# Kernel tuning notes

Hardware: AMD Instinct MI355X
Metric: run time of the kernel (lower is better)

Reference implementation:

```python
import jax, jax.numpy as jnp
import numpy as np

EPS_BN = 1e-5
EPS_NORM = 1e-12
TOP_K = 512


def _conv(x, w):
    # NCHW conv, stride 1, SAME padding (ultralytics Conv autopad)
    return jax.lax.conv_general_dilated(x, w, (1, 1), 'SAME',
                                        dimension_numbers=('NCHW', 'OIHW', 'NCHW'))


def _bn(x, g, b, m, v):
    # inference-mode BatchNorm2d
    inv = jax.lax.rsqrt(v + EPS_BN)
    return (x - m[None, :, None, None]) * (g * inv)[None, :, None, None] + b[None, :, None, None]


def _descriptor(feat, p):
    (w_dr, g_dr, b_dr, m_dr, v_dr,
     w_d1, g_d1, b_d1, m_d1, v_d1,
     g_e, b_e, m_e, v_e,
     w_d2, g_d2, b_d2, m_d2, v_d2) = p
    # dim_reduce: Conv(channel, channel//2, 1) = conv+BN+SiLU
    x = jax.nn.silu(_bn(_conv(feat, w_dr), g_dr, b_dr, m_dr, v_dr))
    # descriptor: Conv(c/2, c/2, 3) + BN + ReLU + Conv(c/2, c/4, 1)
    x = jax.nn.silu(_bn(_conv(x, w_d1), g_d1, b_d1, m_d1, v_d1))
    x = jax.nn.relu(_bn(x, g_e, b_e, m_e, v_e))
    x = jax.nn.silu(_bn(_conv(x, w_d2), g_d2, b_d2, m_d2, v_d2))
    return x


def _keypoints(desc):
    b, c, h, w = desc.shape
    resp = jnp.sqrt(jnp.sum(desc * desc, axis=1)).reshape(b, h * w)  # L2 norm over channels
    _, idx = jax.lax.top_k(resp, TOP_K)                              # [b, K]
    y = (idx // w).astype(desc.dtype) / (h - 1) * 2 - 1
    x = (idx % w).astype(desc.dtype) / (w - 1) * 2 - 1
    return jnp.stack([x, y], axis=-1), idx                           # [b,K,2], [b,K]


def _forward(rgb_feat, ir_feat, params):
    rgb_desc = _descriptor(rgb_feat, params)
    ir_desc = _descriptor(ir_feat, params)

    kp1, idx1 = _keypoints(rgb_desc)
    kp2, idx2 = _keypoints(ir_desc)

    b, c, h, w = rgb_desc.shape
    hw = h * w
    d1 = rgb_desc.reshape(b, c, hw)
    d2 = ir_desc.reshape(b, c, hw)
    d1 = d1 / jnp.maximum(jnp.linalg.norm(d1, axis=1, keepdims=True), EPS_NORM)
    d2 = d2 / jnp.maximum(jnp.linalg.norm(d2, axis=1, keepdims=True), EPS_NORM)
    corr = jnp.einsum('bcn,bcm->bnm', d1, d2)     # [b, hw, hw]
    soft = jax.nn.softmax(corr, axis=-1)

    # scalar matching weight per keypoint pair (gather at keypoint locations)
    bidx = jnp.arange(b)[:, None]
    wts = soft[bidx, idx1, idx2]                  # [b, K]

    # vectorized DLT: A rows, two per point, weighted
    x1, y1 = kp1[..., 0], kp1[..., 1]
    x2, y2 = kp2[..., 0], kp2[..., 1]
    one = jnp.ones_like(x1)
    zer = jnp.zeros_like(x1)
    r1 = jnp.stack([x1, y1, one, zer, zer, zer, -x2 * x1, -x2 * y1, -x2], axis=-1)
    r2 = jnp.stack([zer, zer, zer, x1, y1, one, -y2 * x1, -y2 * y1, -y2], axis=-1)
    A = jnp.stack([r1, r2], axis=2) * wts[:, :, None, None]   # [b,K,2,9]
    A = A.reshape(b, 2 * TOP_K, 9)

    _, _, Vh = jnp.linalg.svd(A, full_matrices=False)          # Vh: [b,9,9]
    # torch.svd returns V; original takes V[-1] == last COLUMN of jax Vh
    H = Vh[:, :, -1].reshape(b, 3, 3)
    return H, rgb_desc, ir_desc


def setup_inputs() -> dict:
    key = jax.random.key(0)
    ks = jax.random.split(key, 8)
    B, C, Hh, Ww = 2, 256, 64, 64
    c2, c4 = C // 2, C // 4
    f32 = jnp.float32

    def bn_params(c):
        return (jnp.ones((c,), f32), jnp.zeros((c,), f32),
                jnp.zeros((c,), f32), jnp.ones((c,), f32))

    g_dr, b_dr, m_dr, v_dr = bn_params(c2)
    g_d1, b_d1, m_d1, v_d1 = bn_params(c2)
    g_e, b_e, m_e, v_e = bn_params(c2)
    g_d2, b_d2, m_d2, v_d2 = bn_params(c4)

    return {
        'rgb_feat': jax.random.normal(ks[0], (B, C, Hh, Ww), f32),
        'ir_feat': jax.random.normal(ks[1], (B, C, Hh, Ww), f32),
        'w_dr': jax.random.normal(ks[2], (c2, C, 1, 1), f32) * 0.05,
        'g_dr': g_dr, 'b_dr': b_dr, 'm_dr': m_dr, 'v_dr': v_dr,
        'w_d1': jax.random.normal(ks[3], (c2, c2, 3, 3), f32) * 0.05,
        'g_d1': g_d1, 'b_d1': b_d1, 'm_d1': m_d1, 'v_d1': v_d1,
        'g_e': g_e, 'b_e': b_e, 'm_e': m_e, 'v_e': v_e,
        'w_d2': jax.random.normal(ks[4], (c4, c2, 1, 1), f32) * 0.05,
        'g_d2': g_d2, 'b_d2': b_d2, 'm_d2': m_d2, 'v_d2': v_d2,
    }


def reference(rgb_feat, ir_feat,
              w_dr, g_dr, b_dr, m_dr, v_dr,
              w_d1, g_d1, b_d1, m_d1, v_d1,
              g_e, b_e, m_e, v_e,
              w_d2, g_d2, b_d2, m_d2, v_d2):
    params = (w_dr, g_dr, b_dr, m_dr, v_dr,
              w_d1, g_d1, b_d1, m_d1, v_d1,
              g_e, b_e, m_e, v_e,
              w_d2, g_d2, b_d2, m_d2, v_d2)
    return _forward(rgb_feat, ir_feat, params)
```

## Files before the change

### kernel.cpp

```cpp
#include <hip/hip_runtime.h>
#include <math.h>


#define HW4 4096
#define NIMG 4

#define OFF_X1   0L
#define OFF_X2   (OFF_X1 + 4L*128*4096)
#define OFF_RESP (OFF_X2 + 4L*128*4096)
#define OFF_INVN (OFF_RESP + 4L*4096)
#define OFF_TOPI (OFF_INVN + 4L*4096)
#define OFF_WTS  (OFF_TOPI + 4L*512)
#define OFF_A    (OFF_WTS + 2L*512)
#define OFF_QN   OFF_X1
#define OFF_PART (OFF_X1 + 65536L)

#define NSPLIT 16

__device__ __forceinline__ float silu_f(float y) { return y / (1.f + expf(-y)); }

__global__ __launch_bounds__(256) void fm_conv1(
    const float* __restrict__ rgb, const float* __restrict__ ir,
    const float* __restrict__ w, const float* __restrict__ g,
    const float* __restrict__ bb, const float* __restrict__ mm,
    const float* __restrict__ vv, float* __restrict__ x1) {
  __shared__ float wl[256*8];
  int bid = blockIdx.x;
  int pblk = bid & 3, ocg = (bid >> 2) & 15, img = bid >> 6;
  int oc0 = ocg * 8;
  int tid = threadIdx.x;
  const float* src = (img < 2) ? (rgb + (long)img*256*HW4) : (ir + (long)(img-2)*256*HW4);
  for (int i = tid; i < 2048; i += 256) {
    int o = i & 7, ic = i >> 3;
    wl[i] = w[(oc0 + o)*256 + ic];
  }
  __syncthreads();
  int p0 = pblk*1024 + tid*4;
  float acc[8][4];
  #pragma unroll
  for (int o = 0; o < 8; ++o)
    #pragma unroll
    for (int j = 0; j < 4; ++j) acc[o][j] = 0.f;
  #pragma unroll 4
  for (int ic = 0; ic < 256; ++ic) {
    float4 v = *(const float4*)(src + (long)ic*HW4 + p0);
    float4 wa = *(const float4*)&wl[ic*8];
    float4 wb = *(const float4*)&wl[ic*8 + 4];
    acc[0][0] = fmaf(wa.x, v.x, acc[0][0]); acc[0][1] = fmaf(wa.x, v.y, acc[0][1]);
    acc[0][2] = fmaf(wa.x, v.z, acc[0][2]); acc[0][3] = fmaf(wa.x, v.w, acc[0][3]);
    acc[1][0] = fmaf(wa.y, v.x, acc[1][0]); acc[1][1] = fmaf(wa.y, v.y, acc[1][1]);
    acc[1][2] = fmaf(wa.y, v.z, acc[1][2]); acc[1][3] = fmaf(wa.y, v.w, acc[1][3]);
    acc[2][0] = fmaf(wa.z, v.x, acc[2][0]); acc[2][1] = fmaf(wa.z, v.y, acc[2][1]);
    acc[2][2] = fmaf(wa.z, v.z, acc[2][2]); acc[2][3] = fmaf(wa.z, v.w, acc[2][3]);
    acc[3][0] = fmaf(wa.w, v.x, acc[3][0]); acc[3][1] = fmaf(wa.w, v.y, acc[3][1]);
    acc[3][2] = fmaf(wa.w, v.z, acc[3][2]); acc[3][3] = fmaf(wa.w, v.w, acc[3][3]);
    acc[4][0] = fmaf(wb.x, v.x, acc[4][0]); acc[4][1] = fmaf(wb.x, v.y, acc[4][1]);
    acc[4][2] = fmaf(wb.x, v.z, acc[4][2]); acc[4][3] = fmaf(wb.x, v.w, acc[4][3]);
    acc[5][0] = fmaf(wb.y, v.x, acc[5][0]); acc[5][1] = fmaf(wb.y, v.y, acc[5][1]);
    acc[5][2] = fmaf(wb.y, v.z, acc[5][2]); acc[5][3] = fmaf(wb.y, v.w, acc[5][3]);
    acc[6][0] = fmaf(wb.z, v.x, acc[6][0]); acc[6][1] = fmaf(wb.z, v.y, acc[6][1]);
    acc[6][2] = fmaf(wb.z, v.z, acc[6][2]); acc[6][3] = fmaf(wb.z, v.w, acc[6][3]);
    acc[7][0] = fmaf(wb.w, v.x, acc[7][0]); acc[7][1] = fmaf(wb.w, v.y, acc[7][1]);
    acc[7][2] = fmaf(wb.w, v.z, acc[7][2]); acc[7][3] = fmaf(wb.w, v.w, acc[7][3]);
  }
  #pragma unroll
  for (int o = 0; o < 8; ++o) {
    int oc = oc0 + o;
    float inv = 1.f / sqrtf(vv[oc] + 1e-5f);
    float sc = g[oc]*inv;
    float4 r;
    r.x = silu_f((acc[o][0] - mm[oc])*sc + bb[oc]);
    r.y = silu_f((acc[o][1] - mm[oc])*sc + bb[oc]);
    r.z = silu_f((acc[o][2] - mm[oc])*sc + bb[oc]);
    r.w = silu_f((acc[o][3] - mm[oc])*sc + bb[oc]);
    *(float4*)(x1 + ((long)img*128 + oc)*HW4 + p0) = r;
  }
}

#define C3_TW 72
#define C3_TR 18
__global__ __launch_bounds__(256) void fm_conv3(
    const float* __restrict__ x1, const float* __restrict__ w,
    const float* __restrict__ g1, const float* __restrict__ b1,
    const float* __restrict__ m1, const float* __restrict__ v1,
    const float* __restrict__ ge, const float* __restrict__ be,
    const float* __restrict__ me, const float* __restrict__ ve,
    float* __restrict__ x2) {
  __shared__ float t[2][4][C3_TR*C3_TW];
  __shared__ float wl[2][4][9][8];
  int bid = blockIdx.x;
  int rt = bid & 3, ocg = (bid >> 2) & 15, img = bid >> 6;
  int oc0 = ocg * 8;
  int y0 = rt * 16;
  int tid = threadIdx.x;
  int ly = tid >> 4;
  int lx = tid & 15;
  int x0 = lx * 4;
  const float* xim = x1 + (long)img*128*HW4;

  int gbase[5][4];
  int lofs[5];
  #pragma unroll
  for (int t5 = 0; t5 < 5; ++t5) {
    int i = tid + 256*t5;
    if (i < 1224) {
      int q = i / 306, r = i - q*306;
      int row = r / 17, seg = r - row*17;
      int gy = y0 + row - 1;
      lofs[t5] = q*(C3_TR*C3_TW) + row*C3_TW + 4 + seg*4;
      #pragma unroll
      for (int e = 0; e < 4; ++e) {
        int x = seg*4 + e - 1;
        gbase[t5][e] = (gy >= 0 && gy < 64 && x >= 0 && x < 64)
                       ? (q*HW4 + gy*64 + x) : -1;
      }
    } else {
      lofs[t5] = -1;
      #pragma unroll
      for (int e = 0; e < 4; ++e) gbase[t5][e] = -1;
    }
  }
  int wg0 = -1, wl0 = 0, wg1 = -1, wl1 = 0;
  {
    int i = tid;
    if (i < 288) {
      int o = i & 7, k = (i >> 3) % 9, q = i / 72;
      wg0 = ((oc0 + o)*128 + q)*9 + k;
      wl0 = (q*9 + k)*8 + o;
    }
    i = tid + 256;
    if (i < 288) {
      int o = i & 7, k = (i >> 3) % 9, q = i / 72;
      wg1 = ((oc0 + o)*128 + q)*9 + k;
      wl1 = (q*9 + k)*8 + o;
    }
  }

  float4 sreg[5];
  float wreg0 = 0.f, wreg1 = 0.f;

  #define C3_LOAD(IC0) do {                                              \
    long icoff = (long)(IC0)*HW4;                                        \
    _Pragma("unroll")                                                    \
    for (int t5 = 0; t5 < 5; ++t5) {                                     \
      sreg[t5].x = (gbase[t5][0] >= 0) ? xim[icoff + gbase[t5][0]] : 0.f;\
      sreg[t5].y = (gbase[t5][1] >= 0) ? xim[icoff + gbase[t5][1]] : 0.f;\
      sreg[t5].z = (gbase[t5][2] >= 0) ? xim[icoff + gbase[t5][2]] : 0.f;\
      sreg[t5].w = (gbase[t5][3] >= 0) ? xim[icoff + gbase[t5][3]] : 0.f;\
    }                                                                    \
    if (wg0 >= 0) wreg0 = w[(long)(IC0)*9 + wg0];                        \
    if (wg1 >= 0) wreg1 = w[(long)(IC0)*9 + wg1];                        \
  } while (0)

  #define C3_WRITE(BUF) do {                                             \
    float* tb = &t[BUF][0][0];                                           \
    _Pragma("unroll")                                                    \
    for (int t5 = 0; t5 < 5; ++t5)                                       \
      if (lofs[t5] >= 0) *(float4*)(tb + lofs[t5]) = sreg[t5];           \
    if (wg0 >= 0) (&wl[BUF][0][0][0])[wl0] = wreg0;                      \
    if (wg1 >= 0) (&wl[BUF][0][0][0])[wl1] = wreg1;                      \
  } while (0)

  float acc[8][4];
  #pragma unroll
  for (int o = 0; o < 8; ++o)
    #pragma unroll
    for (int j = 0; j < 4; ++j) acc[o][j] = 0.f;

  C3_LOAD(0);
  C3_WRITE(0);
  __syncthreads();
  int pb = 0;
  for (int ic0 = 0; ic0 < 128; ic0 += 4) {
    if (ic0 + 4 < 128) C3_LOAD(ic0 + 4);
    #pragma unroll
    for (int q = 0; q < 4; ++q) {
      const float* tq = &t[pb][q][0];
      float n6[3][6];
      #pragma unroll
      for (int dy = 0; dy < 3; ++dy) {
        float4 a = *(const float4*)(tq + (ly + dy)*C3_TW + x0 + 4);
        float4 b2 = *(const float4*)(tq + (ly + dy)*C3_TW + x0 + 8);
        n6[dy][0] = a.x; n6[dy][1] = a.y; n6[dy][2] = a.z;
        n6[dy][3] = a.w; n6[dy][4] = b2.x; n6[dy][5] = b2.y;
      }
      #pragma unroll
      for (int k = 0; k < 9; ++k) {
        const int dy = k / 3, dx = k % 3;
        float4 wA = *(const float4*)&wl[pb][q][k][0];
        float4 wB = *(const float4*)&wl[pb][q][k][4];
        #pragma unroll
        for (int j = 0; j < 4; ++j) {
          float nv = n6[dy][dx + j];
          acc[0][j] = fmaf(wA.x, nv, acc[0][j]);
          acc[1][j] = fmaf(wA.y, nv, acc[1][j]);
          acc[2][j] = fmaf(wA.z, nv, acc[2][j]);
          acc[3][j] = fmaf(wA.w, nv, acc[3][j]);
          acc[4][j] = fmaf(wB.x, nv, acc[4][j]);
          acc[5][j] = fmaf(wB.y, nv, acc[5][j]);
          acc[6][j] = fmaf(wB.z, nv, acc[6][j]);
          acc[7][j] = fmaf(wB.w, nv, acc[7][j]);
        }
      }
    }
    if (ic0 + 4 < 128) C3_WRITE(pb ^ 1);
    __syncthreads();
    pb ^= 1;
  }
  int prow = (y0 + ly)*64 + x0;
  #pragma unroll
  for (int o = 0; o < 8; ++o) {
    int oc = oc0 + o;
    float inv1 = 1.f / sqrtf(v1[oc] + 1e-5f);
    float s1 = g1[oc]*inv1;
    float inve = 1.f / sqrtf(ve[oc] + 1e-5f);
    float s2 = ge[oc]*inve;
    float4 r;
    float y;
    y = silu_f((acc[o][0] - m1[oc])*s1 + b1[oc]); r.x = fmaxf((y - me[oc])*s2 + be[oc], 0.f);
    y = silu_f((acc[o][1] - m1[oc])*s1 + b1[oc]); r.y = fmaxf((y - me[oc])*s2 + be[oc], 0.f);
    y = silu_f((acc[o][2] - m1[oc])*s1 + b1[oc]); r.z = fmaxf((y - me[oc])*s2 + be[oc], 0.f);
    y = silu_f((acc[o][3] - m1[oc])*s1 + b1[oc]); r.w = fmaxf((y - me[oc])*s2 + be[oc], 0.f);
    *(float4*)(x2 + ((long)img*128 + oc)*HW4 + prow) = r;
  }
}

__global__ __launch_bounds__(256) void fm_conv2(
    const float* __restrict__ x2, const float* __restrict__ w,
    const float* __restrict__ g, const float* __restrict__ bb,
    const float* __restrict__ mm, const float* __restrict__ vv,
    float* __restrict__ out) {
  __shared__ float wl[128*4];
  int bid = blockIdx.x;
  int pblk = bid & 3, ocg = (bid >> 2) & 15, img = bid >> 6;
  int oc0 = ocg * 4;
  int tid = threadIdx.x;
  for (int i = tid; i < 512; i += 256) {
    int o = i & 3, ic = i >> 2;
    wl[i] = w[(oc0 + o)*128 + ic];
  }
  __syncthreads();
  int p0 = pblk*1024 + tid*4;
  const float* src = x2 + (long)img*128*HW4;
  float acc[4][4];
  #pragma unroll
  for (int o = 0; o < 4; ++o)
    #pragma unroll
    for (int j = 0; j < 4; ++j) acc[o][j] = 0.f;
  #pragma unroll 4
  for (int ic = 0; ic < 128; ++ic) {
    float4 v = *(const float4*)(src + (long)ic*HW4 + p0);
    float4 wa = *(const float4*)&wl[ic*4];
    acc[0][0] = fmaf(wa.x, v.x, acc[0][0]); acc[0][1] = fmaf(wa.x, v.y, acc[0][1]);
    acc[0][2] = fmaf(wa.x, v.z, acc[0][2]); acc[0][3] = fmaf(wa.x, v.w, acc[0][3]);
    acc[1][0] = fmaf(wa.y, v.x, acc[1][0]); acc[1][1] = fmaf(wa.y, v.y, acc[1][1]);
    acc[1][2] = fmaf(wa.y, v.z, acc[1][2]); acc[1][3] = fmaf(wa.y, v.w, acc[1][3]);
    acc[2][0] = fmaf(wa.z, v.x, acc[2][0]); acc[2][1] = fmaf(wa.z, v.y, acc[2][1]);
    acc[2][2] = fmaf(wa.z, v.z, acc[2][2]); acc[2][3] = fmaf(wa.z, v.w, acc[2][3]);
    acc[3][0] = fmaf(wa.w, v.x, acc[3][0]); acc[3][1] = fmaf(wa.w, v.y, acc[3][1]);
    acc[3][2] = fmaf(wa.w, v.z, acc[3][2]); acc[3][3] = fmaf(wa.w, v.w, acc[3][3]);
  }
  #pragma unroll
  for (int o = 0; o < 4; ++o) {
    int oc = oc0 + o;
    float inv = 1.f / sqrtf(vv[oc] + 1e-5f);
    float sc = g[oc]*inv;
    float* dst = out + 18 + (long)img*262144 + (long)oc*HW4 + p0;
    #pragma unroll
    for (int j = 0; j < 4; ++j)
      dst[j] = silu_f((acc[o][j] - mm[oc])*sc + bb[oc]);
  }
}

__global__ __launch_bounds__(256) void fm_resp(
    const float* __restrict__ out, float* __restrict__ resp, float* __restrict__ invn) {
  int t = blockIdx.x*256 + threadIdx.x;
  if (t >= NIMG*HW4) return;
  int img = t >> 12, p = t & 4095;
  const float* d = out + 18 + (long)img*262144;
  float s = 0.f;
  #pragma unroll
  for (int c = 0; c < 64; ++c) { float x = d[c*HW4 + p]; s = fmaf(x, x, s); }
  float r = sqrtf(s);
  resp[t] = r;
  invn[t] = 1.f / fmaxf(r, 1e-12f);
}

__global__ __launch_bounds__(1024) void fm_sort(
    const float* __restrict__ resp, int* __restrict__ topidx) {
  __shared__ unsigned long long keys[4096];
  int img = blockIdx.x, tid = threadIdx.x;
  const float* r = resp + (long)img*HW4;
  for (int i = tid; i < 4096; i += 1024) {
    unsigned int vb = __float_as_uint(r[i]);
    keys[i] = ((unsigned long long)vb << 32) | (unsigned int)(4095 - i);
  }
  __syncthreads();
  for (int k = 2; k <= 4096; k <<= 1) {
    for (int j = k >> 1; j > 0; j >>= 1) {
      for (int t = tid; t < 2048; t += 1024) {
        int i = 2*t - (t & (j - 1));
        int ixj = i ^ j;
        bool up = ((i & k) == 0);
        unsigned long long a = keys[i], b = keys[ixj];
        if ((a < b) == up) { keys[i] = b; keys[ixj] = a; }
      }
      __syncthreads();
    }
  }
  if (tid < 512) topidx[img*512 + tid] = 4095 - (int)(keys[tid] & 0xFFFFFFFFull);
}

__global__ __launch_bounds__(256) void fm_qgather(
    const float* __restrict__ out, const float* __restrict__ invn,
    const int* __restrict__ topidx, float* __restrict__ qn) {
  int tid = threadIdx.x;
  int kp = blockIdx.x*4 + (tid >> 6);
  int c = tid & 63;
  int b = kp >> 9, k = kp & 511;
  int row = topidx[b*512 + k];
  const float* d1 = out + 18 + (long)b*262144;
  qn[(long)kp*64 + c] = d1[c*HW4 + row] * invn[(long)b*HW4 + row];
}

__global__ __launch_bounds__(256) void fm_corr(
    const float* __restrict__ out, const float* __restrict__ invn,
    const float* __restrict__ qn, float* __restrict__ part) {
  __shared__ float Qs[32*64];
  __shared__ float Ds[64*128];
  int tid = threadIdx.x;
  int tx = tid & 31, ty = tid >> 5;
  int jsplit = blockIdx.x;
  int kg = blockIdx.y;
  int b = blockIdx.z;
  int k0 = kg*32;
  const float* d2 = out + 18 + (long)(2 + b)*262144;
  const float* in2 = invn + (long)(2 + b)*HW4;
  {
    const float4* src = (const float4*)(qn + ((long)b*512 + k0)*64);
    float4* dst = (float4*)Qs;
    dst[tid] = src[tid];
    dst[tid + 256] = src[tid + 256];
  }
  float m[4], s[4];
  #pragma unroll
  for (int r = 0; r < 4; ++r) { m[r] = -INFINITY; s[r] = 0.f; }
  #pragma unroll
  for (int tile = 0; tile < 2; ++tile) {
    int j0 = jsplit*256 + tile*128;
    __syncthreads();
    {
      float4* dst = (float4*)Ds;
      #pragma unroll
      for (int t = 0; t < 8; ++t) {
        int i = tid + 256*t;
        int c = i >> 5, col4 = i & 31;
        dst[i] = *(const float4*)(d2 + (long)c*HW4 + j0 + col4*4);
      }
    }
    __syncthreads();
    float acc[4][4];
    #pragma unroll
    for (int r = 0; r < 4; ++r)
      #pragma unroll
      for (int cc = 0; cc < 4; ++cc) acc[r][cc] = 0.f;
    const float4* Ds4 = (const float4*)Ds;
    #pragma unroll 4
    for (int c = 0; c < 64; ++c) {
      float4 dv = Ds4[c*32 + tx];
      #pragma unroll
      for (int r = 0; r < 4; ++r) {
        float qv = Qs[(ty*4 + r)*64 + c];
        acc[r][0] = fmaf(qv, dv.x, acc[r][0]);
        acc[r][1] = fmaf(qv, dv.y, acc[r][1]);
        acc[r][2] = fmaf(qv, dv.z, acc[r][2]);
        acc[r][3] = fmaf(qv, dv.w, acc[r][3]);
      }
    }
    float i0 = in2[j0 + tx*4 + 0];
    float i1 = in2[j0 + tx*4 + 1];
    float i2 = in2[j0 + tx*4 + 2];
    float i3 = in2[j0 + tx*4 + 3];
    #pragma unroll
    for (int r = 0; r < 4; ++r) {
      float v0 = acc[r][0]*i0, v1 = acc[r][1]*i1, v2 = acc[r][2]*i2, v3 = acc[r][3]*i3;
      float vm = fmaxf(fmaxf(v0, v1), fmaxf(v2, v3));
      float nm = fmaxf(m[r], vm);
      s[r] = s[r]*expf(m[r] - nm) + expf(v0 - nm) + expf(v1 - nm) + expf(v2 - nm) + expf(v3 - nm);
      m[r] = nm;
    }
  }
  #pragma unroll
  for (int off = 1; off < 32; off <<= 1) {
    #pragma unroll
    for (int r = 0; r < 4; ++r) {
      float om = __shfl_xor(m[r], off);
      float os = __shfl_xor(s[r], off);
      float nm = fmaxf(m[r], om);
      s[r] = s[r]*expf(m[r] - nm) + os*expf(om - nm);
      m[r] = nm;
    }
  }
  if (tx == 0) {
    #pragma unroll
    for (int r = 0; r < 4; ++r) {
      long idx = (((long)b*512 + k0 + ty*4 + r)*NSPLIT + jsplit)*2;
      part[idx] = m[r];
      part[idx + 1] = s[r];
    }
  }
}

__global__ __launch_bounds__(256) void fm_comb(
    const float* __restrict__ out, const float* __restrict__ invn,
    const int* __restrict__ topidx, const float* __restrict__ qn,
    const float* __restrict__ part, float* __restrict__ wts) {
  int tid = threadIdx.x;
  int kp = blockIdx.x*4 + (tid >> 6);
  int lane = tid & 63;
  int b = kp >> 9, k = kp & 511;
  int col = topidx[(2 + b)*512 + k];
  const float* d2 = out + 18 + (long)(2 + b)*262144;
  float dot = qn[(long)kp*64 + lane] * d2[lane*HW4 + col];
  #pragma unroll
  for (int off = 1; off < 64; off <<= 1) dot += __shfl_xor(dot, off);
  if (lane == 0) {
    const float* pp = part + (long)kp*NSPLIT*2;
    float M = -INFINITY;
    #pragma unroll
    for (int i = 0; i < NSPLIT; ++i) M = fmaxf(M, pp[2*i]);
    float S = 0.f;
    #pragma unroll
    for (int i = 0; i < NSPLIT; ++i) S += pp[2*i + 1]*expf(pp[2*i] - M);
    float v = dot * invn[(long)(2 + b)*HW4 + col];
    wts[b*512 + k] = expf(v - M)/S;
  }
}

__global__ __launch_bounds__(256) void fm_build(
    const int* __restrict__ topidx, const float* __restrict__ wts,
    float* __restrict__ A) {
  int t = blockIdx.x*256 + threadIdx.x;
  if (t >= 1024) return;
  int b = t >> 9, k = t & 511;
  int i1 = topidx[b*512 + k], i2 = topidx[(2 + b)*512 + k];
  float w = wts[b*512 + k];
  float x1 = (float)(i1 & 63) / 63.f * 2.f - 1.f;
  float y1 = (float)(i1 >> 6) / 63.f * 2.f - 1.f;
  float x2 = (float)(i2 & 63) / 63.f * 2.f - 1.f;
  float y2 = (float)(i2 >> 6) / 63.f * 2.f - 1.f;
  float* r = A + ((long)b*1024 + 2*k)*9;
  r[0] = x1*w;  r[1] = y1*w;  r[2] = w;
  r[3] = 0.f;   r[4] = 0.f;   r[5] = 0.f;
  r[6] = (-x2*x1)*w; r[7] = (-x2*y1)*w; r[8] = (-x2)*w;
  r[9]  = 0.f;  r[10] = 0.f;  r[11] = 0.f;
  r[12] = x1*w; r[13] = y1*w; r[14] = w;
  r[15] = (-y2*x1)*w; r[16] = (-y2*y1)*w; r[17] = (-y2)*w;
}

__device__ __forceinline__ void lap_slartg(float f, float g, float* cs, float* sn, float* r) {
  if (g == 0.f) { *cs = 1.f; *sn = 0.f; *r = f; }
  else if (f == 0.f) { *cs = 0.f; *sn = copysignf(1.f, g); *r = fabsf(g); }
  else {
    float d = sqrtf(f*f + g*g);
    *cs = fabsf(f) / d;
    *r = copysignf(d, f);
    *sn = g / (*r);
  }
}

__device__ __forceinline__ void lap_slas2(float f, float g, float h, float* ssmin, float* ssmax) {
  float fa = fabsf(f), ga = fabsf(g), ha = fabsf(h);
  float fhmn = fminf(fa, ha), fhmx = fmaxf(fa, ha);
  if (fhmn == 0.f) {
    *ssmin = 0.f;
    if (fhmx == 0.f) *ssmax = ga;
    else {
      float mx = fmaxf(fhmx, ga), mn = fminf(fhmx, ga);
      float q = mn / mx;
      *ssmax = mx * sqrtf(1.f + q*q);
    }
  } else {
    if (ga < fhmx) {
      float as_ = 1.f + fhmn/fhmx;
      float at_ = (fhmx - fhmn)/fhmx;
      float au = ga/fhmx; au = au*au;
      float c = 2.f / (sqrtf(as_*as_ + au) + sqrtf(at_*at_ + au));
      *ssmin = fhmn*c;
      *ssmax = fhmx/c;
    } else {
      float au = fhmx/ga;
      if (au == 0.f) { *ssmin = (fhmn*fhmx)/ga; *ssmax = ga; }
      else {
        float as_ = 1.f + fhmn/fhmx;
        float at_ = (fhmx - fhmn)/fhmx;
        float t1 = as_*au, t2 = at_*au;
        float c = 1.f / (sqrtf(1.f + t1*t1) + sqrtf(1.f + t2*t2));
        float smn = (fhmn*c)*au;
        *ssmin = smn + smn;
        *ssmax = ga/(c + c);
      }
    }
  }
}

__device__ __forceinline__ void lap_slasv2(float f, float g, float h, float* ssmin, float* ssmax,
                           float* snr, float* csr, float* snl, float* csl) {
  const float epsv = 5.9604645e-08f;
  float ft = f, fa = fabsf(f), ht = h, ha = fabsf(h);
  int pmax = 1;
  bool swap_ = (ha > fa);
  if (swap_) { pmax = 3; float tmp = ft; ft = ht; ht = tmp; tmp = fa; fa = ha; ha = tmp; }
  float gt = g, ga = fabsf(gt);
  float clt = 0.f, crt = 0.f, slt = 0.f, srt = 0.f;
  if (ga == 0.f) { *ssmin = ha; *ssmax = fa; clt = 1.f; crt = 1.f; slt = 0.f; srt = 0.f; }
  else {
    bool gasmal = true;
    if (ga > fa) {
      pmax = 2;
      if ((fa/ga) < epsv) {
        gasmal = false;
        *ssmax = ga;
        if (ha > 1.f) *ssmin = fa/(ga/ha); else *ssmin = (fa/ga)*ha;
        clt = 1.f; slt = ht/gt; srt = 1.f; crt = ft/gt;
      }
    }
    if (gasmal) {
      float d = fa - ha, l;
      if (d == fa) l = 1.f; else l = d/fa;
      float m_ = gt/ft;
      float t = 2.f - l;
      float mm2 = m_*m_, tt = t*t;
      float s = sqrtf(tt + mm2);
      float r_ = (l == 0.f) ? fabsf(m_) : sqrtf(l*l + mm2);
      float a = 0.5f*(s + r_);
      *ssmin = ha/a;
      *ssmax = fa*a;
      if (mm2 == 0.f) {
        if (l == 0.f) t = copysignf(2.f, ft)*copysignf(1.f, gt);
        else t = gt/copysignf(d, ft) + m_/t;
      } else {
        t = (m_/(s + t) + m_/(r_ + l))*(1.f + a);
      }
      float l2 = sqrtf(t*t + 4.f);
      crt = 2.f/l2;
      srt = t/l2;
      clt = (crt + srt*m_)/a;
      slt = (ht/ft)*srt/a;
    }
  }
  if (swap_) { *csl = srt; *snl = crt; *csr = slt; *snr = clt; }
  else { *csl = clt; *snl = slt; *csr = crt; *snr = srt; }
  float tsign = 1.f;
  if (pmax == 1) tsign = copysignf(1.f, *csr)*copysignf(1.f, *csl)*copysignf(1.f, f);
  if (pmax == 2) tsign = copysignf(1.f, *snr)*copysignf(1.f, *csl)*copysignf(1.f, g);
  if (pmax == 3) tsign = copysignf(1.f, *snr)*copysignf(1.f, *snl)*copysignf(1.f, h);
  *ssmax = copysignf(*ssmax, tsign);
  *ssmin = copysignf(*ssmin, tsign*copysignf(1.f, f)*copysignf(1.f, h));
}

__device__ __forceinline__ float get9(const float (&a)[9], int idx) {
  float v = a[0];
#pragma unroll
  for (int i = 1; i < 9; ++i) if (idx == i) v = a[i];
  return v;
}
__device__ __forceinline__ void set9(float (&a)[9], int idx, float val) {
#pragma unroll
  for (int i = 0; i < 9; ++i) if (idx == i) a[i] = val;
}

__device__ __forceinline__ void bdsqr9_reg(float (&dd)[9], float (&ee)[9], float (&vt)[9]) {
  const float eps_ = 5.9604645e-08f;
  const float unfl_ = 1.17549435e-38f;
  const float tol_ = 10.f*eps_;
  float sminoa = fabsf(dd[0]);
  if (sminoa != 0.f) {
    float mu = sminoa;
    bool z = false;
#pragma unroll
    for (int i = 1; i < 9; ++i) {
      if (!z) {
        mu = fabsf(dd[i])*(mu/(mu + fabsf(ee[i-1])));
        sminoa = fminf(sminoa, mu);
        if (sminoa == 0.f) z = true;
      }
    }
  }
  sminoa = sminoa / 3.f;
  float thresh = fmaxf(tol_*sminoa, 486.f*unfl_);
  int m = 9, iter = 0, oldll = -1, oldm = -1, idir = 0;
  float sminl = 0.f;
  int guard = 0;
  while (guard++ < 2000) {
    if (m <= 1) break;
    if (iter > 486) break;
    float smax = fabsf(get9(dd, m-1));
    int ll = 0; bool split = false;
#pragma unroll
    for (int l2 = 8; l2 >= 1; --l2) {
      if (l2 <= m - 1 && !split) {
        float abss = fabsf(dd[l2-1]);
        float abse = fabsf(ee[l2-1]);
        if (abse <= thresh) { ll = l2; split = true; }
        else smax = fmaxf(smax, fmaxf(abss, abse));
      }
    }
    if (split) {
      set9(ee, ll-1, 0.f);
      if (ll == m - 1) { m = m - 1; continue; }
    } else ll = 0;
    ll = ll + 1;
    if (ll == m - 1) {
      float d1 = get9(dd, m-2), e1 = get9(ee, m-2), d2v = get9(dd, m-1);
      float sigmn, sigmx, sinr, cosr, sinl_, cosl_;
      lap_slasv2(d1, e1, d2v, &sigmn, &sigmx, &sinr, &cosr, &sinl_, &cosl_);
      set9(dd, m-2, sigmx); set9(ee, m-2, 0.f); set9(dd, m-1, sigmn);
      float xt = get9(vt, m-2), yt = get9(vt, m-1);
      set9(vt, m-2, cosr*xt + sinr*yt);
      set9(vt, m-1, cosr*yt - sinr*xt);
      m -= 2; continue;
    }
    if (ll > oldm || m < oldll)
      idir = (fabsf(get9(dd, ll-1)) >= fabsf(get9(dd, m-1))) ? 1 : 2;
    bool conv = false;
    if (idir == 1) {
      if (fabsf(get9(ee, m-2)) <= tol_*fabsf(get9(dd, m-1))) { set9(ee, m-2, 0.f); continue; }
      float mu = fabsf(get9(dd, ll-1));
      sminl = mu;
#pragma unroll
      for (int lll = 1; lll <= 8; ++lll) {
        if (lll >= ll && lll <= m - 1 && !conv) {
          if (fabsf(ee[lll-1]) <= tol_*mu) { ee[lll-1] = 0.f; conv = true; }
          else {
            mu = fabsf(dd[lll])*(mu/(mu + fabsf(ee[lll-1])));
            sminl = fminf(sminl, mu);
          }
        }
      }
    } else {
      if (fabsf(get9(ee, ll-1)) <= tol_*fabsf(get9(dd, ll-1))) { set9(ee, ll-1, 0.f); continue; }
      float mu = fabsf(get9(dd, m-1));
      sminl = mu;
#pragma unroll
      for (int lll = 8; lll >= 1; --lll) {
        if (lll <= m - 1 && lll >= ll && !conv) {
          if (fabsf(ee[lll-1]) <= tol_*mu) { ee[lll-1] = 0.f; conv = true; }
          else {
            mu = fabsf(dd[lll-1])*(mu/(mu + fabsf(ee[lll-1])));
            sminl = fminf(sminl, mu);
          }
        }
      }
    }
    if (conv) continue;
    oldll = ll; oldm = m;
    float shift = 0.f, rdum;
    if (!(9.f*tol_*(sminl/smax) <= fmaxf(eps_, 0.01f*tol_))) {
      float sll;
      if (idir == 1) { sll = fabsf(get9(dd, ll-1)); lap_slas2(get9(dd, m-2), get9(ee, m-2), get9(dd, m-1), &shift, &rdum); }
      else           { sll = fabsf(get9(dd, m-1));  lap_slas2(get9(dd, ll-1), get9(ee, ll-1), get9(dd, ll), &shift, &rdum); }
      if (sll > 0.f) { float q = shift/sll; if (q*q < eps_) shift = 0.f; }
    }
    iter += m - ll;
    if (shift == 0.f) {
      if (idir == 1) {
        float cs = 1.f, oldcs = 1.f, sn = 0.f, oldsn = 0.f, r;
#pragma unroll
        for (int i = 1; i <= 8; ++i) {
          if (i >= ll && i <= m - 1) {
            lap_slartg(dd[i-1]*cs, ee[i-1], &cs, &sn, &r);
            if (i >= 2 && i > ll) ee[i-2] = oldsn*r;
            float dn;
            lap_slartg(oldcs*r, dd[i]*sn, &oldcs, &oldsn, &dn);
            dd[i-1] = dn;
            float t = vt[i]; vt[i] = cs*t - sn*vt[i-1]; vt[i-1] = sn*t + cs*vt[i-1];
          }
        }
        float h2 = get9(dd, m-1)*cs;
        set9(dd, m-1, h2*oldcs);
        set9(ee, m-2, h2*oldsn);
        if (fabsf(get9(ee, m-2)) <= thresh) set9(ee, m-2, 0.f);
      } else {
        float cs = 1.f, oldcs = 1.f, sn = 0.f, oldsn = 0.f, r;
#pragma unroll
        for (int i = 9; i >= 2; --i) {
          if (i <= m && i >= ll + 1) {
            lap_slartg(dd[i-1]*cs, ee[i-2], &cs, &sn, &r);
            if (i < m) ee[i-1] = oldsn*r;
            float dn;
            lap_slartg(oldcs*r, dd[i-2]*sn, &oldcs, &oldsn, &dn);
            dd[i-1] = dn;
            float c2 = oldcs, s2 = -oldsn;
            float t = vt[i-1]; vt[i-1] = c2*t - s2*vt[i-2]; vt[i-2] = s2*t + c2*vt[i-2];
          }
        }
        float h2 = get9(dd, ll-1)*cs;
        set9(dd, ll-1, h2*oldcs);
        set9(ee, ll-1, h2*oldsn);
        if (fabsf(get9(ee, ll-1)) <= thresh) set9(ee, ll-1, 0.f);
      }
    } else {
      if (idir == 1) {
        float d0 = get9(dd, ll-1);
        float f2 = (fabsf(d0) - shift)*(copysignf(1.f, d0) + shift/d0);
        float g2 = get9(ee, ll-1);
#pragma unroll
        for (int i = 1; i <= 8; ++i) {
          if (i >= ll && i <= m - 1) {
            float cr, sr, cl, sl, r;
            lap_slartg(f2, g2, &cr, &sr, &r);
            if (i >= 2 && i > ll) ee[i-2] = r;
            f2 = cr*dd[i-1] + sr*ee[i-1];
            ee[i-1] = cr*ee[i-1] - sr*dd[i-1];
            g2 = sr*dd[i];
            dd[i] = cr*dd[i];
            lap_slartg(f2, g2, &cl, &sl, &r);
            dd[i-1] = r;
            f2 = cl*ee[i-1] + sl*dd[i];
            dd[i] = cl*dd[i] - sl*ee[i-1];
            if (i < m - 1) { g2 = sl*ee[i]; ee[i] = cl*ee[i]; }
            float t = vt[i]; vt[i] = cr*t - sr*vt[i-1]; vt[i-1] = sr*t + cr*vt[i-1];
          }
        }
        set9(ee, m-2, f2);
        if (fabsf(get9(ee, m-2)) <= thresh) set9(ee, m-2, 0.f);
      } else {
        float dm = get9(dd, m-1);
        float f2 = (fabsf(dm) - shift)*(copysignf(1.f, dm) + shift/dm);
        float g2 = get9(ee, m-2);
#pragma unroll
        for (int i = 9; i >= 2; --i) {
          if (i <= m && i >= ll + 1) {
            float cr, sr, cl, sl, r;
            lap_slartg(f2, g2, &cr, &sr, &r);
            if (i < m) ee[i-1] = r;
            f2 = cr*dd[i-1] + sr*ee[i-2];
            ee[i-2] = cr*ee[i-2] - sr*dd[i-1];
            g2 = sr*dd[i-2];
            dd[i-2] = cr*dd[i-2];
            lap_slartg(f2, g2, &cl, &sl, &r);
            dd[i-1] = r;
            f2 = cl*ee[i-2] + sl*dd[i-2];
            dd[i-2] = cl*dd[i-2] - sl*ee[i-2];
            if (i >= 3 && i > ll + 1) { g2 = sl*ee[i-3]; ee[i-3] = cl*ee[i-3]; }
            float c2 = cl, s2 = -sl;
            float t = vt[i-1]; vt[i-1] = c2*t - s2*vt[i-2]; vt[i-2] = s2*t + c2*vt[i-2];
          }
        }
        set9(ee, ll-1, f2);
        if (fabsf(get9(ee, ll-1)) <= thresh) set9(ee, ll-1, 0.f);
      }
    }
  }
#pragma unroll
  for (int i = 0; i < 9; ++i) {
    if (dd[i] < 0.f) { dd[i] = -dd[i]; vt[i] = -vt[i]; }
  }
#pragma unroll
  for (int i = 1; i <= 8; ++i) {
    int isub = 1; float smin2 = dd[0];
#pragma unroll
    for (int j = 2; j <= 9; ++j) {
      if (j <= 10 - i) {
        if (dd[j-1] <= smin2) { isub = j; smin2 = dd[j-1]; }
      }
    }
    const int tgt = 10 - i;
    if (isub != tgt) {
      set9(dd, isub-1, dd[tgt-1]);
      dd[tgt-1] = smin2;
      float tv = get9(vt, isub-1);
      set9(vt, isub-1, vt[tgt-1]);
      vt[tgt-1] = tv;
    }
  }
}

__global__ __launch_bounds__(256) void fm_svd(
    const float* __restrict__ Aglob, float* __restrict__ outH) {
  __shared__ float As[1024*9];
  __shared__ float wred[4][12];
  __shared__ float bc[4];
  int b = blockIdx.x, tid = threadIdx.x;
  int wv = tid >> 6, ln = tid & 63;
  const float* Ab = Aglob + (long)b*9216;
  {
    const float4* s4 = (const float4*)Ab;
    float4* d4 = (float4*)As;
#pragma unroll
    for (int t = 0; t < 9; ++t) d4[tid + 256*t] = s4[tid + 256*t];
  }
  __syncthreads();
  for (int k = 0; k < 9; ++k) {
    float ps = 0.f;
    for (int r = k + 1 + tid; r < 1024; r += 256) {
      float x = As[r*9 + k]; ps = fmaf(x, x, ps);
    }
#pragma unroll
    for (int off = 1; off < 64; off <<= 1) ps += __shfl_xor(ps, off);
    if (ln == 0) wred[wv][8] = ps;
    __syncthreads();
    if (tid == 0) {
      float ssq = wred[0][8] + wred[1][8] + wred[2][8] + wred[3][8];
      float alpha = As[k*9 + k];
      float tau = 0.f, sc = 0.f, beta = alpha;
      if (ssq != 0.f) {
        beta = -copysignf(sqrtf(alpha*alpha + ssq), alpha);
        tau = (beta - alpha)/beta;
        sc = 1.f/(alpha - beta);
      }
      bc[0] = tau; bc[1] = sc; bc[2] = beta;
    }
    __syncthreads();
    float tau = bc[0], sc = bc[1];
    if (tau != 0.f) {
      for (int r = k + 1 + tid; r < 1024; r += 256) As[r*9 + k] *= sc;
    }
    __syncthreads();
    if (tau != 0.f) {
      float pd[8];
#pragma unroll
      for (int jj = 0; jj < 8; ++jj) pd[jj] = 0.f;
      for (int r = k + 1 + tid; r < 1024; r += 256) {
        float vk = As[r*9 + k];
#pragma unroll
        for (int jj = 0; jj < 8; ++jj) {
          int j = k + 1 + jj;
          if (j < 9) pd[jj] = fmaf(vk, As[r*9 + j], pd[jj]);
        }
      }
#pragma unroll
      for (int off = 1; off < 64; off <<= 1) {
#pragma unroll
        for (int jj = 0; jj < 8; ++jj) pd[jj] += __shfl_xor(pd[jj], off);
      }
      if (ln == 0) {
#pragma unroll
        for (int jj = 0; jj < 8; ++jj) wred[wv][jj] = pd[jj];
      }
      __syncthreads();
      float sj[8];
#pragma unroll
      for (int jj = 0; jj < 8; ++jj) {
        int j = k + 1 + jj;
        float v = 0.f;
        if (j < 9)
          v = (wred[0][jj] + wred[1][jj] + wred[2][jj] + wred[3][jj] + As[k*9 + j]) * tau;
        sj[jj] = v;
      }
      for (int r = k + 1 + tid; r < 1024; r += 256) {
        float vk = As[r*9 + k];
#pragma unroll
        for (int jj = 0; jj < 8; ++jj) {
          int j = k + 1 + jj;
          if (j < 9) As[r*9 + j] -= sj[jj]*vk;
        }
      }
      __syncthreads();
      if (tid == 0) {
#pragma unroll
        for (int jj = 0; jj < 8; ++jj) {
          int j = k + 1 + jj;
          if (j < 9) As[k*9 + j] -= sj[jj];
        }
      }
    }
    if (tid == 0) As[k*9 + k] = bc[2];
    __syncthreads();
  }
  if (tid < 64) {
    float R[9][9];
#pragma unroll
    for (int i = 0; i < 9; ++i)
#pragma unroll
      for (int j = 0; j < 9; ++j)
        R[i][j] = (j >= i) ? As[i*9 + j] : 0.f;
    float dd[9], ee[9], taupv[8], pt8[9];
    ee[8] = 0.f;
#pragma unroll
    for (int i = 0; i < 9; ++i) {
      float alpha = R[i][i];
      float ssq = 0.f;
#pragma unroll
      for (int r2 = i + 1; r2 < 9; ++r2) ssq += R[r2][i]*R[r2][i];
      float tauq = 0.f, beta = alpha;
      if (ssq != 0.f) {
        beta = -copysignf(sqrtf(alpha*alpha + ssq), alpha);
        tauq = (beta - alpha)/beta;
        float scq = 1.f/(alpha - beta);
#pragma unroll
        for (int r2 = i + 1; r2 < 9; ++r2) R[r2][i] *= scq;
      }
      dd[i] = beta;
      if (tauq != 0.f) {
#pragma unroll
        for (int j = i + 1; j < 9; ++j) {
          float s = R[i][j];
#pragma unroll
          for (int r2 = i + 1; r2 < 9; ++r2) s += R[r2][i]*R[r2][j];
          s *= tauq;
          R[i][j] -= s;
#pragma unroll
          for (int r2 = i + 1; r2 < 9; ++r2) R[r2][j] -= s*R[r2][i];
        }
      }
      if (i < 8) {
        float alpha2 = R[i][i+1];
        float ssq2 = 0.f;
#pragma unroll
        for (int c = i + 2; c < 9; ++c) ssq2 += R[i][c]*R[i][c];
        float tp = 0.f, beta2 = alpha2;
        if (ssq2 != 0.f) {
          beta2 = -copysignf(sqrtf(alpha2*alpha2 + ssq2), alpha2);
          tp = (beta2 - alpha2)/beta2;
          float scp = 1.f/(alpha2 - beta2);
#pragma unroll
          for (int c = i + 2; c < 9; ++c) R[i][c] *= scp;
        }
        ee[i] = beta2;
        taupv[i] = tp;
        if (tp != 0.f) {
#pragma unroll
          for (int r2 = i + 1; r2 < 9; ++r2) {
            float s = R[r2][i+1];
#pragma unroll
            for (int c = i + 2; c < 9; ++c) s += R[i][c]*R[r2][c];
            s *= tp;
            R[r2][i+1] -= s;
#pragma unroll
            for (int c = i + 2; c < 9; ++c) R[r2][c] -= s*R[i][c];
          }
        }
      }
    }
#pragma unroll
    for (int i = 0; i < 9; ++i) pt8[i] = (i == 8) ? 1.f : 0.f;
#pragma unroll
    for (int i = 0; i < 8; ++i) {
      float tp = taupv[i];
      if (tp != 0.f) {
        float s = pt8[i+1];
#pragma unroll
        for (int r2 = i + 2; r2 < 9; ++r2) s += R[i][r2]*pt8[r2];
        s *= tp;
        pt8[i+1] -= s;
#pragma unroll
        for (int r2 = i + 2; r2 < 9; ++r2) pt8[r2] -= s*R[i][r2];
      }
    }
    float vt[9];
#pragma unroll
    for (int i = 0; i < 9; ++i) vt[i] = (i == tid) ? 1.f : 0.f;
    bdsqr9_reg(dd, ee, vt);
    float p8 = (tid < 9) ? get9(pt8, tid) : 0.f;
    float h[9];
#pragma unroll
    for (int i = 0; i < 9; ++i) h[i] = vt[i]*p8;
#pragma unroll
    for (int off = 1; off < 16; off <<= 1) {
#pragma unroll
      for (int i = 0; i < 9; ++i) h[i] += __shfl_xor(h[i], off);
    }
    if (tid == 0) {
#pragma unroll
      for (int i = 0; i < 9; ++i) outH[b*9 + i] = h[i];
    }
  }
}

extern "C" void kernel_launch(void* const* d_in, const int* in_sizes, int n_in,
                              void* d_out, int out_size, void* d_ws, size_t ws_size,
                              hipStream_t stream) {
  const float* rgb  = (const float*)d_in[0];
  const float* ir   = (const float*)d_in[1];
  const float* w_dr = (const float*)d_in[2];
  const float* g_dr = (const float*)d_in[3];
  const float* b_dr = (const float*)d_in[4];
  const float* m_dr = (const float*)d_in[5];
  const float* v_dr = (const float*)d_in[6];
  const float* w_d1 = (const float*)d_in[7];
  const float* g_d1 = (const float*)d_in[8];
  const float* b_d1 = (const float*)d_in[9];
  const float* m_d1 = (const float*)d_in[10];
  const float* v_d1 = (const float*)d_in[11];
  const float* g_e  = (const float*)d_in[12];
  const float* b_e  = (const float*)d_in[13];
  const float* m_e  = (const float*)d_in[14];
  const float* v_e  = (const float*)d_in[15];
  const float* w_d2 = (const float*)d_in[16];
  const float* g_d2 = (const float*)d_in[17];
  const float* b_d2 = (const float*)d_in[18];
  const float* m_d2 = (const float*)d_in[19];
  const float* v_d2 = (const float*)d_in[20];

  float* out = (float*)d_out;
  float* ws  = (float*)d_ws;
  float* x1   = ws + OFF_X1;
  float* x2   = ws + OFF_X2;
  float* resp = ws + OFF_RESP;
  float* invn = ws + OFF_INVN;
  int*   topi = (int*)(ws + OFF_TOPI);
  float* wts  = ws + OFF_WTS;
  float* Amat = ws + OFF_A;
  float* qn   = ws + OFF_QN;
  float* part = ws + OFF_PART;

  fm_conv1<<<256, 256, 0, stream>>>(rgb, ir, w_dr, g_dr, b_dr, m_dr, v_dr, x1);
  fm_conv3<<<256, 256, 0, stream>>>(x1, w_d1, g_d1, b_d1, m_d1, v_d1,
                                    g_e, b_e, m_e, v_e, x2);
  fm_conv2<<<256, 256, 0, stream>>>(x2, w_d2, g_d2, b_d2, m_d2, v_d2, out);
  fm_resp<<<(NIMG*HW4 + 255)/256, 256, 0, stream>>>(out, resp, invn);
  fm_sort<<<NIMG, 1024, 0, stream>>>(resp, topi);
  fm_qgather<<<256, 256, 0, stream>>>(out, invn, topi, qn);
  fm_corr<<<dim3(NSPLIT, 16, 2), 256, 0, stream>>>(out, invn, qn, part);
  fm_comb<<<256, 256, 0, stream>>>(out, invn, topi, qn, part, wts);
  fm_build<<<4, 256, 0, stream>>>(topi, wts, Amat);
  fm_svd<<<2, 256, 0, stream>>>(Amat, out);
}
```

Baseline: 385.3 us.

## Fuse response, top-k sort and query gather; fold DLT build into combine

Merges the per-pixel norm computation, bitonic top-k sort and query-descriptor gather into one kernel running one block per image, and folds the DLT row construction into the softmax combine kernel. This cuts three kernel launches and the round trips through global memory for the response and weight buffers. The bitonic sort now does its last two merge stages (j=2,1) inside registers, four keys per thread, which saves barriers. The cost is that the norm reduction now runs on only 4 blocks instead of 64, so far less of the GPU is busy during that phase.

Measured after the change: 432.4 us (median of 3 runs). 12.2% more time.

```diff
diff --git a/kernel.cpp b/kernel.cpp
--- a/kernel.cpp
+++ b/kernel.cpp
@@ -272,32 +272,25 @@
   }
 }
 
-__global__ __launch_bounds__(256) void fm_resp(
-    const float* __restrict__ out, float* __restrict__ resp, float* __restrict__ invn) {
-  int t = blockIdx.x*256 + threadIdx.x;
-  if (t >= NIMG*HW4) return;
-  int img = t >> 12, p = t & 4095;
-  const float* d = out + 18 + (long)img*262144;
-  float s = 0.f;
-  #pragma unroll
-  for (int c = 0; c < 64; ++c) { float x = d[c*HW4 + p]; s = fmaf(x, x, s); }
-  float r = sqrtf(s);
-  resp[t] = r;
-  invn[t] = 1.f / fmaxf(r, 1e-12f);
-}
-
-__global__ __launch_bounds__(1024) void fm_sort(
-    const float* __restrict__ resp, int* __restrict__ topidx) {
+__global__ __launch_bounds__(1024) void fm_sortf(
+    const float* __restrict__ out, float* __restrict__ invn,
+    int* __restrict__ topidx, float* __restrict__ qn) {
   __shared__ unsigned long long keys[4096];
   int img = blockIdx.x, tid = threadIdx.x;
-  const float* r = resp + (long)img*HW4;
-  for (int i = tid; i < 4096; i += 1024) {
-    unsigned int vb = __float_as_uint(r[i]);
-    keys[i] = ((unsigned long long)vb << 32) | (unsigned int)(4095 - i);
+  const float* d = out + 18 + (long)img*262144;
+  #pragma unroll
+  for (int q = 0; q < 4; ++q) {
+    int p = tid + q*1024;
+    float s = 0.f;
+    #pragma unroll
+    for (int c = 0; c < 64; ++c) { float x = d[c*HW4 + p]; s = fmaf(x, x, s); }
+    float r = sqrtf(s);
+    invn[(long)img*HW4 + p] = 1.f / fmaxf(r, 1e-12f);
+    keys[p] = ((unsigned long long)__float_as_uint(r) << 32) | (unsigned int)(4095 - p);
   }
   __syncthreads();
   for (int k = 2; k <= 4096; k <<= 1) {
-    for (int j = k >> 1; j > 0; j >>= 1) {
+    for (int j = k >> 1; j >= 4; j >>= 1) {
       for (int t = tid; t < 2048; t += 1024) {
         int i = 2*t - (t & (j - 1));
         int ixj = i ^ j;
@@ -307,20 +300,35 @@
       }
       __syncthreads();
     }
+    {
+      int base = tid << 2;
+      unsigned long long e0 = keys[base], e1 = keys[base+1];
+      unsigned long long e2 = keys[base+2], e3 = keys[base+3];
+      if (k == 2) {
+        if (e0 < e1)  { unsigned long long t_ = e0; e0 = e1; e1 = t_; }
+        if (e2 >= e3) { unsigned long long t_ = e2; e2 = e3; e3 = t_; }
+      } else {
+        bool up = ((base & k) == 0);
+        if ((e0 < e2) == up) { unsigned long long t_ = e0; e0 = e2; e2 = t_; }
+        if ((e1 < e3) == up) { unsigned long long t_ = e1; e1 = e3; e3 = t_; }
+        if ((e0 < e1) == up) { unsigned long long t_ = e0; e0 = e1; e1 = t_; }
+        if ((e2 < e3) == up) { unsigned long long t_ = e2; e2 = e3; e3 = t_; }
+      }
+      keys[base] = e0; keys[base+1] = e1; keys[base+2] = e2; keys[base+3] = e3;
+    }
+    __syncthreads();
   }
   if (tid < 512) topidx[img*512 + tid] = 4095 - (int)(keys[tid] & 0xFFFFFFFFull);
-}
-
-__global__ __launch_bounds__(256) void fm_qgather(
-    const float* __restrict__ out, const float* __restrict__ invn,
-    const int* __restrict__ topidx, float* __restrict__ qn) {
-  int tid = threadIdx.x;
-  int kp = blockIdx.x*4 + (tid >> 6);
-  int c = tid & 63;
-  int b = kp >> 9, k = kp & 511;
-  int row = topidx[b*512 + k];
-  const float* d1 = out + 18 + (long)b*262144;
-  qn[(long)kp*64 + c] = d1[c*HW4 + row] * invn[(long)b*HW4 + row];
+  if (img < 2) {
+    for (int e = tid; e < 512*64; e += 1024) {
+      int k = e >> 6, c = e & 63;
+      unsigned long long key = keys[k];
+      int row = 4095 - (int)(key & 0xFFFFFFFFull);
+      float r = __uint_as_float((unsigned int)(key >> 32));
+      float iv = 1.f / fmaxf(r, 1e-12f);
+      qn[((long)img*512 + k)*64 + c] = d[c*HW4 + row] * iv;
+    }
+  }
 }
 
 __global__ __launch_bounds__(256) void fm_corr(
@@ -414,7 +422,7 @@
 __global__ __launch_bounds__(256) void fm_comb(
     const float* __restrict__ out, const float* __restrict__ invn,
     const int* __restrict__ topidx, const float* __restrict__ qn,
-    const float* __restrict__ part, float* __restrict__ wts) {
+    const float* __restrict__ part, float* __restrict__ A) {
   int tid = threadIdx.x;
   int kp = blockIdx.x*4 + (tid >> 6);
   int lane = tid & 63;
@@ -433,29 +441,20 @@
     #pragma unroll
     for (int i = 0; i < NSPLIT; ++i) S += pp[2*i + 1]*expf(pp[2*i] - M);
     float v = dot * invn[(long)(2 + b)*HW4 + col];
-    wts[b*512 + k] = expf(v - M)/S;
-  }
-}
-
-__global__ __launch_bounds__(256) void fm_build(
-    const int* __restrict__ topidx, const float* __restrict__ wts,
-    float* __restrict__ A) {
-  int t = blockIdx.x*256 + threadIdx.x;
-  if (t >= 1024) return;
-  int b = t >> 9, k = t & 511;
-  int i1 = topidx[b*512 + k], i2 = topidx[(2 + b)*512 + k];
-  float w = wts[b*512 + k];
-  float x1 = (float)(i1 & 63) / 63.f * 2.f - 1.f;
-  float y1 = (float)(i1 >> 6) / 63.f * 2.f - 1.f;
-  float x2 = (float)(i2 & 63) / 63.f * 2.f - 1.f;
-  float y2 = (float)(i2 >> 6) / 63.f * 2.f - 1.f;
-  float* r = A + ((long)b*1024 + 2*k)*9;
-  r[0] = x1*w;  r[1] = y1*w;  r[2] = w;
-  r[3] = 0.f;   r[4] = 0.f;   r[5] = 0.f;
-  r[6] = (-x2*x1)*w; r[7] = (-x2*y1)*w; r[8] = (-x2)*w;
-  r[9]  = 0.f;  r[10] = 0.f;  r[11] = 0.f;
-  r[12] = x1*w; r[13] = y1*w; r[14] = w;
-  r[15] = (-y2*x1)*w; r[16] = (-y2*y1)*w; r[17] = (-y2)*w;
+    float wt = expf(v - M)/S;
+    int i1 = topidx[b*512 + k];
+    float x1 = (float)(i1 & 63) / 63.f * 2.f - 1.f;
+    float y1 = (float)(i1 >> 6) / 63.f * 2.f - 1.f;
+    float x2 = (float)(col & 63) / 63.f * 2.f - 1.f;
+    float y2 = (float)(col >> 6) / 63.f * 2.f - 1.f;
+    float* r = A + ((long)b*1024 + 2*k)*9;
+    r[0] = x1*wt;  r[1] = y1*wt;  r[2] = wt;
+    r[3] = 0.f;    r[4] = 0.f;    r[5] = 0.f;
+    r[6] = (-x2*x1)*wt; r[7] = (-x2*y1)*wt; r[8] = (-x2)*wt;
+    r[9]  = 0.f;   r[10] = 0.f;   r[11] = 0.f;
+    r[12] = x1*wt; r[13] = y1*wt; r[14] = wt;
+    r[15] = (-y2*x1)*wt; r[16] = (-y2*y1)*wt; r[17] = (-y2)*wt;
+  }
 }
 
 __device__ __forceinline__ void lap_slartg(float f, float g, float* cs, float* sn, float* r) {
@@ -998,10 +997,8 @@
   float* ws  = (float*)d_ws;
   float* x1   = ws + OFF_X1;
   float* x2   = ws + OFF_X2;
-  float* resp = ws + OFF_RESP;
   float* invn = ws + OFF_INVN;
   int*   topi = (int*)(ws + OFF_TOPI);
-  float* wts  = ws + OFF_WTS;
   float* Amat = ws + OFF_A;
   float* qn   = ws + OFF_QN;
   float* part = ws + OFF_PART;
@@ -1010,11 +1007,8 @@
   fm_conv3<<<256, 256, 0, stream>>>(x1, w_d1, g_d1, b_d1, m_d1, v_d1,
                                     g_e, b_e, m_e, v_e, x2);
   fm_conv2<<<256, 256, 0, stream>>>(x2, w_d2, g_d2, b_d2, m_d2, v_d2, out);
-  fm_resp<<<(NIMG*HW4 + 255)/256, 256, 0, stream>>>(out, resp, invn);
-  fm_sort<<<NIMG, 1024, 0, stream>>>(resp, topi);
-  fm_qgather<<<256, 256, 0, stream>>>(out, invn, topi, qn);
+  fm_sortf<<<NIMG, 1024, 0, stream>>>(out, invn, topi, qn);
   fm_corr<<<dim3(NSPLIT, 16, 2), 256, 0, stream>>>(out, invn, qn, part);
-  fm_comb<<<256, 256, 0, stream>>>(out, invn, topi, qn, part, wts);
-  fm_build<<<4, 256, 0, stream>>>(topi, wts, Amat);
+  fm_comb<<<256, 256, 0, stream>>>(out, invn, topi, qn, part, Amat);
   fm_svd<<<2, 256, 0, stream>>>(Amat, out);
 }
```
